# Kernel tuning notes

Hardware: AMD Instinct MI355X
Metric: run time of the kernel (lower is better)

The kernel has to match this reference:

```python
import jax, jax.numpy as jnp
import numpy as np

N_NODES = 50000
N_EDGES = 800000
F_IN, HID, N_CLS = 128, 64, 40
KS = 2  # kernel_size, dim=1, open B-spline, degree=1


def spline_conv(x, src, dst, pseudo, W, root, bias, num_nodes, kernel_size):
    """SplineConv (torch_geometric), dim=1, degree=1, open spline, aggr='mean'."""
    K = kernel_size
    v = pseudo[:, 0] * (K - 1)                       # map [0,1] -> [0, K-1]
    k0 = jnp.clip(jnp.floor(v), 0, K - 2)
    frac = v - k0                                    # linear (degree-1) basis
    i0 = k0.astype(jnp.int32)
    i1 = i0 + 1
    E = src.shape[0]
    e = jnp.arange(E)
    # per-edge kernel coefficients c[e,k] = sum_s basis[e,s]*[idx[e,s]==k]
    c = jnp.zeros((E, K), x.dtype).at[e, i0].add(1.0 - frac).at[e, i1].add(frac)
    xj = x[src]                                      # [E, F_in] gather
    # agg[k] = scatter-add over edges of c[e,k]*xj[e] -> [K, N, F_in]
    agg = jnp.stack([
        jax.ops.segment_sum(c[:, k:k + 1] * xj, dst, num_segments=num_nodes)
        for k in range(K)
    ])
    deg = jax.ops.segment_sum(jnp.ones((E,), x.dtype), dst, num_segments=num_nodes)
    msg = jnp.einsum('kni,kio->no', agg, W) / jnp.maximum(deg, 1.0)[:, None]
    return msg + x @ root + bias


def setup_inputs() -> dict:
    key = jax.random.key(0)
    ks = jax.random.split(key, 9)
    def glorot(k, shape):
        fan_in, fan_out = shape[-2], shape[-1]
        lim = (6.0 / (fan_in + fan_out)) ** 0.5
        return jax.random.uniform(k, shape, jnp.float32, -lim, lim)
    return {
        'x': jax.random.normal(ks[0], (N_NODES, F_IN), jnp.float32),
        'edge_index': jax.random.randint(ks[1], (2, N_EDGES), 0, N_NODES, jnp.int32),
        'edge_attr': jax.random.uniform(ks[2], (N_EDGES, 1), jnp.float32),
        'W1': glorot(ks[3], (KS, F_IN, HID)),
        'root1': glorot(ks[4], (F_IN, HID)),
        'bias1': jnp.zeros((HID,), jnp.float32),
        'W2': glorot(ks[5], (KS, HID, N_CLS)),
        'root2': glorot(ks[6], (HID, N_CLS)),
        'bias2': jnp.zeros((N_CLS,), jnp.float32),
    }


def reference(x, edge_index, edge_attr, W1, root1, bias1, W2, root2, bias2):
    src, dst = edge_index[0], edge_index[1]
    # eval mode: dropout is identity
    h = spline_conv(x, src, dst, edge_attr, W1, root1, bias1, N_NODES, KS)
    h = jax.nn.elu(h)
    out = spline_conv(h, src, dst, edge_attr, W2, root2, bias2, N_NODES, KS)
    return out
```

## Files before the change

### kernel.cpp

```cpp
#include <hip/hip_runtime.h>
#include <math.h>

#define N_NODES 50000
#define N_EDGES 800000
#define F_IN    128
#define HID     64
#define N_CLS   40

#define M1 (3 * HID)
#define M2P 128

#define RANGE_SZ 6250
#define PERM_SLICES 128
#define PERM_CHUNK (N_EDGES / PERM_SLICES)
#define EST 64

#define NW 32768

using sh8 = __attribute__((ext_vector_type(8))) short;
using floatx4 = __attribute__((ext_vector_type(4))) float;

__device__ inline unsigned short f2bf(float f) {
    union { float f; unsigned int u; } c{f};
    unsigned int r = (c.u + 0x7FFF + ((c.u >> 16) & 1)) >> 16;
    return (unsigned short)r;
}
__device__ inline float bf2f(unsigned int u) {
    union { unsigned int u; float f; } c;
    c.u = u << 16;
    return c.f;
}

__global__ void concat_w(const float* __restrict__ W1, const float* __restrict__ root1,
                         const float* __restrict__ W2, const float* __restrict__ root2,
                         unsigned short* __restrict__ WT1, unsigned short* __restrict__ WT2,
                         int* __restrict__ cnt) {
    int i = blockIdx.x * blockDim.x + threadIdx.x;
    if (i < M1 * F_IN) {
        int c = i / F_IN, k = i % F_IN;
        float val;
        if (c < HID)            val = W1[k * HID + c];
        else if (c < 2 * HID)   val = W1[F_IN * HID + k * HID + (c - HID)];
        else                    val = root1[k * HID + (c - 2 * HID)];
        WT1[i] = f2bf(val);
    } else if (i < NW) {
        int ii = i - M1 * F_IN;
        int c = ii / HID, k = ii % HID;
        float val;
        if (c < N_CLS)            val = W2[k * N_CLS + c];
        else if (c < 2 * N_CLS)   val = W2[HID * N_CLS + k * N_CLS + (c - N_CLS)];
        else if (c < 3 * N_CLS)   val = root2[k * N_CLS + (c - 2 * N_CLS)];
        else                      val = 0.0f;
        WT2[ii] = f2bf(val);
    } else {
        int ii = i - NW;
        if (ii < N_NODES) cnt[ii] = 0;
    }
}

template <int KD, bool AF32, int SPLIT, int PW, int ROOTW, int MT>
__device__ __forceinline__ void gemm_body(int bid, const void* __restrict__ Aptr,
                                          const unsigned short* __restrict__ Bt,
                                          unsigned short* __restrict__ Csp,
                                          float* __restrict__ Croot, int Crows) {
    constexpr int KP = KD + 8;
    __shared__ unsigned short As[64 * KP];
    __shared__ unsigned short Bs[64 * KP];

    int tid = threadIdx.x;
    int row0 = bid * 64;

    if (AF32) {
        const float* A = (const float*)Aptr;
        for (int c = tid; c < 64 * (KD / 4); c += 256) {
            int r = c / (KD / 4), q = c % (KD / 4);
            int gr = row0 + r;
            float4 v = make_float4(0.f, 0.f, 0.f, 0.f);
            if (gr < Crows) v = *(const float4*)(A + (size_t)gr * KD + q * 4);
            union { unsigned short s[4]; uint2 u; } pk;
            pk.s[0] = f2bf(v.x); pk.s[1] = f2bf(v.y);
            pk.s[2] = f2bf(v.z); pk.s[3] = f2bf(v.w);
            *(uint2*)&As[r * KP + q * 4] = pk.u;
        }
    } else {
        const unsigned short* A = (const unsigned short*)Aptr;
        for (int c = tid; c < 64 * (KD / 8); c += 256) {
            int r = c / (KD / 8), q = c % (KD / 8);
            int gr = row0 + r;
            sh8 v = {};
            if (gr < Crows) v = *(const sh8*)(A + (size_t)gr * KD + q * 8);
            *(sh8*)&As[r * KP + q * 8] = v;
        }
    }

    int wv = tid >> 6, lane = tid & 63;
    int lrow = lane & 15, lq = lane >> 4;

    for (int mt = 0; mt < MT; ++mt) {
        int c0 = mt * 64;
        __syncthreads();
        for (int c = tid; c < 64 * (KD / 8); c += 256) {
            int r = c / (KD / 8), q = c % (KD / 8);
            *(sh8*)&Bs[r * KP + q * 8] = *(const sh8*)(Bt + (size_t)(c0 + r) * KD + q * 8);
        }
        __syncthreads();

        floatx4 acc[4] = {{0.f,0.f,0.f,0.f},{0.f,0.f,0.f,0.f},{0.f,0.f,0.f,0.f},{0.f,0.f,0.f,0.f}};
#pragma unroll
        for (int kt = 0; kt < KD / 32; ++kt) {
            int kb = kt * 32 + lq * 8;
            sh8 a0 = *(const sh8*)&As[(wv * 16 + lrow) * KP + kb];
#pragma unroll
            for (int cf = 0; cf < 4; ++cf) {
                sh8 b = *(const sh8*)&Bs[(cf * 16 + lrow) * KP + kb];
                acc[cf] = __builtin_amdgcn_mfma_f32_16x16x32_bf16(a0, b, acc[cf], 0, 0, 0);
            }
        }

#pragma unroll
        for (int r = 0; r < 4; ++r) {
            int gr = row0 + wv * 16 + lq * 4 + r;
            if (gr >= Crows) continue;
#pragma unroll
            for (int cf = 0; cf < 4; ++cf) {
                int gc = c0 + cf * 16 + lrow;
                float val = acc[cf][r];
                if (gc < SPLIT) {
                    int pi = (gc < PW) ? gc * 2 : (gc - PW) * 2 + 1;
                    Csp[(size_t)gr * SPLIT + pi] = f2bf(val);
                } else if (gc < SPLIT + ROOTW) {
                    Croot[(size_t)gr * ROOTW + (gc - SPLIT)] = val;
                }
            }
        }
    }
}

__device__ __forceinline__ void permute_body(int b, const int* __restrict__ src,
                                             const int* __restrict__ dst,
                                             const float* __restrict__ attr,
                                             int* __restrict__ cnt,
                                             unsigned int* __restrict__ edata) {
    int range = b & 7;
    int slice = b >> 3;
    int lo = range * RANGE_SZ;
    int e0 = slice * PERM_CHUNK;
    int e1 = e0 + PERM_CHUNK;
    for (int e = e0 + (int)threadIdx.x; e < e1; e += 256) {
        int d = dst[e];
        if ((unsigned)(d - lo) < (unsigned)RANGE_SZ) {
            int pos = atomicAdd(&cnt[d], 1);
            if (pos < EST) {
                unsigned int q = (unsigned int)(attr[e] * 65535.0f + 0.5f);
                edata[d * EST + pos] = (unsigned int)src[e] | (q << 16);
            }
        }
    }
}

__global__ __launch_bounds__(256) void gemm1_permute(const float* __restrict__ x,
                                                     const unsigned short* __restrict__ WT1,
                                                     unsigned short* __restrict__ Ysp,
                                                     float* __restrict__ Yroot,
                                                     const int* __restrict__ src,
                                                     const int* __restrict__ dst,
                                                     const float* __restrict__ attr,
                                                     int* __restrict__ cnt,
                                                     unsigned int* __restrict__ edata,
                                                     int gemmBlocks) {
    if ((int)blockIdx.x < gemmBlocks) {
        gemm_body<128, true, 128, 64, 64, 3>(blockIdx.x, (const void*)x, WT1, Ysp, Yroot, N_NODES);
    } else {
        permute_body(blockIdx.x - gemmBlocks, src, dst, attr, cnt, edata);
    }
}

template <int KD, bool AF32, int SPLIT, int PW, int ROOTW, int MT>
__global__ __launch_bounds__(256) void gemm_mfma(const void* __restrict__ Aptr,
                                                 const unsigned short* __restrict__ Bt,
                                                 unsigned short* __restrict__ Csp,
                                                 float* __restrict__ Croot,
                                                 int Crows) {
    gemm_body<KD, AF32, SPLIT, PW, ROOTW, MT>(blockIdx.x, Aptr, Bt, Csp, Croot, Crows);
}

__global__ __launch_bounds__(256) void gather1(const unsigned short* __restrict__ Ysp,
                                               const float* __restrict__ Yroot,
                                               const int* __restrict__ cnt,
                                               const unsigned int* __restrict__ edata,
                                               const float* __restrict__ bias1,
                                               unsigned short* __restrict__ h) {
    int wave = (blockIdx.x * blockDim.x + threadIdx.x) >> 6;
    int lane = threadIdx.x & 63;
    if (wave >= N_NODES) return;
    int deg = cnt[wave];
    deg = deg > EST ? EST : deg;
    const unsigned int* eb = edata + (size_t)wave * EST;
    const float qs = 1.0f / 65535.0f;
    float acc = 0.0f;
    if (deg <= 16) {
        unsigned int e[16], p[16];
#pragma unroll
        for (int t = 0; t < 16; ++t) e[t] = eb[t];
#pragma unroll
        for (int t = 0; t < 16; ++t) {
            int idx = (t < deg) ? (int)(e[t] & 0xffffu) : 0;
            p[t] = *(const unsigned int*)(Ysp + (size_t)idx * 128 + lane * 2);
        }
#pragma unroll
        for (int t = 0; t < 16; ++t) {
            float m = (t < deg) ? 1.0f : 0.0f;
            float v = (float)(e[t] >> 16) * qs;
            acc += m * ((1.0f - v) * bf2f(p[t] & 0xffffu) + v * bf2f(p[t] >> 16));
        }
    } else {
        unsigned int e[32], p[32];
#pragma unroll
        for (int t = 0; t < 32; ++t) e[t] = eb[t];
#pragma unroll
        for (int t = 0; t < 32; ++t) {
            int idx = (t < deg) ? (int)(e[t] & 0xffffu) : 0;
            p[t] = *(const unsigned int*)(Ysp + (size_t)idx * 128 + lane * 2);
        }
#pragma unroll
        for (int t = 0; t < 32; ++t) {
            float m = (t < deg) ? 1.0f : 0.0f;
            float v = (float)(e[t] >> 16) * qs;
            acc += m * ((1.0f - v) * bf2f(p[t] & 0xffffu) + v * bf2f(p[t] >> 16));
        }
        if (deg > 32) {
            for (int j = 32; j < deg; j += 8) {
                unsigned int e2[8], p2[8];
#pragma unroll
                for (int t = 0; t < 8; ++t) e2[t] = eb[j + t];
#pragma unroll
                for (int t = 0; t < 8; ++t) {
                    int idx = (j + t < deg) ? (int)(e2[t] & 0xffffu) : 0;
                    p2[t] = *(const unsigned int*)(Ysp + (size_t)idx * 128 + lane * 2);
                }
#pragma unroll
                for (int t = 0; t < 8; ++t) {
                    float m = (j + t < deg) ? 1.0f : 0.0f;
                    float v = (float)(e2[t] >> 16) * qs;
                    acc += m * ((1.0f - v) * bf2f(p2[t] & 0xffffu) + v * bf2f(p2[t] >> 16));
                }
            }
        }
    }
    float dg = (float)deg;
    dg = dg > 1.0f ? dg : 1.0f;
    float m = acc / dg + Yroot[(size_t)wave * HID + lane] + bias1[lane];
    m = m > 0.0f ? m : expm1f(m);
    h[(size_t)wave * HID + lane] = f2bf(m);
}

__global__ __launch_bounds__(256) void gather2(const unsigned short* __restrict__ Zsp,
                                               const float* __restrict__ Zroot,
                                               const int* __restrict__ cnt,
                                               const unsigned int* __restrict__ edata,
                                               const float* __restrict__ bias2,
                                               float* __restrict__ out) {
    int wave = (blockIdx.x * blockDim.x + threadIdx.x) >> 6;
    int lane = threadIdx.x & 63;
    if (wave >= N_NODES) return;
    if (lane >= N_CLS) return;
    int deg = cnt[wave];
    deg = deg > EST ? EST : deg;
    const unsigned int* eb = edata + (size_t)wave * EST;
    const float qs = 1.0f / 65535.0f;
    float acc = 0.0f;
    if (deg <= 16) {
        unsigned int e[16], p[16];
#pragma unroll
        for (int t = 0; t < 16; ++t) e[t] = eb[t];
#pragma unroll
        for (int t = 0; t < 16; ++t) {
            int idx = (t < deg) ? (int)(e[t] & 0xffffu) : 0;
            p[t] = *(const unsigned int*)(Zsp + (size_t)idx * 80 + lane * 2);
        }
#pragma unroll
        for (int t = 0; t < 16; ++t) {
            float m = (t < deg) ? 1.0f : 0.0f;
            float v = (float)(e[t] >> 16) * qs;
            acc += m * ((1.0f - v) * bf2f(p[t] & 0xffffu) + v * bf2f(p[t] >> 16));
        }
    } else {
        unsigned int e[32], p[32];
#pragma unroll
        for (int t = 0; t < 32; ++t) e[t] = eb[t];
#pragma unroll
        for (int t = 0; t < 32; ++t) {
            int idx = (t < deg) ? (int)(e[t] & 0xffffu) : 0;
            p[t] = *(const unsigned int*)(Zsp + (size_t)idx * 80 + lane * 2);
        }
#pragma unroll
        for (int t = 0; t < 32; ++t) {
            float m = (t < deg) ? 1.0f : 0.0f;
            float v = (float)(e[t] >> 16) * qs;
            acc += m * ((1.0f - v) * bf2f(p[t] & 0xffffu) + v * bf2f(p[t] >> 16));
        }
        if (deg > 32) {
            for (int j = 32; j < deg; j += 8) {
                unsigned int e2[8], p2[8];
#pragma unroll
                for (int t = 0; t < 8; ++t) e2[t] = eb[j + t];
#pragma unroll
                for (int t = 0; t < 8; ++t) {
                    int idx = (j + t < deg) ? (int)(e2[t] & 0xffffu) : 0;
                    p2[t] = *(const unsigned int*)(Zsp + (size_t)idx * 80 + lane * 2);
                }
#pragma unroll
                for (int t = 0; t < 8; ++t) {
                    float m = (j + t < deg) ? 1.0f : 0.0f;
                    float v = (float)(e2[t] >> 16) * qs;
                    acc += m * ((1.0f - v) * bf2f(p2[t] & 0xffffu) + v * bf2f(p2[t] >> 16));
                }
            }
        }
    }
    float dg = (float)deg;
    dg = dg > 1.0f ? dg : 1.0f;
    out[(size_t)wave * N_CLS + lane] =
        acc / dg + Zroot[(size_t)wave * N_CLS + lane] + bias2[lane];
}

extern "C" void kernel_launch(void* const* d_in, const int* in_sizes, int n_in,
                              void* d_out, int out_size, void* d_ws, size_t ws_size,
                              hipStream_t stream) {
    const float* x     = (const float*)d_in[0];
    const int*   eidx  = (const int*)d_in[1];
    const float* eattr = (const float*)d_in[2];
    const float* W1    = (const float*)d_in[3];
    const float* root1 = (const float*)d_in[4];
    const float* bias1 = (const float*)d_in[5];
    const float* W2    = (const float*)d_in[6];
    const float* root2 = (const float*)d_in[7];
    const float* bias2 = (const float*)d_in[8];
    float* out = (float*)d_out;

    const int* src = eidx;
    const int* dst = eidx + N_EDGES;

    char* base = (char*)d_ws;
    unsigned short* Ysp   = (unsigned short*)base;
    float*          Yroot = (float*)(base + 12800000);
    unsigned short* hb    = (unsigned short*)(base + 25600000);
    unsigned short* WT1   = (unsigned short*)(base + 32000000);
    unsigned short* WT2   = (unsigned short*)(base + 32049152);
    unsigned int*   edata = (unsigned int*)(base + 32065536);
    int*            cnt   = (int*)(base + 44865536);
    unsigned short* Zsp   = Ysp;
    float*          Zroot = Yroot;

    const int GB = (N_NODES + 63) / 64;

    hipLaunchKernelGGL(concat_w, dim3((NW + N_NODES + 255) / 256), dim3(256), 0, stream,
                       W1, root1, W2, root2, WT1, WT2, cnt);

    hipLaunchKernelGGL(gemm1_permute, dim3(GB + 8 * PERM_SLICES), dim3(256), 0, stream,
                       x, WT1, Ysp, Yroot, src, dst, eattr, cnt, edata, GB);
    hipLaunchKernelGGL(gather1, dim3((N_NODES * 64 + 255) / 256), dim3(256), 0, stream,
                       Ysp, Yroot, cnt, edata, bias1, hb);

    hipLaunchKernelGGL((gemm_mfma<64, false, 80, 40, 40, 2>),
                       dim3(GB), dim3(256), 0, stream,
                       (const void*)hb, WT2, Zsp, Zroot, N_NODES);
    hipLaunchKernelGGL(gather2, dim3((N_NODES * 64 + 255) / 256), dim3(256), 0, stream,
                       Zsp, Zroot, cnt, edata, bias2, out);
}
```

Measured before the change: 205.2 us.

## Move edge permute into weight-concat kernel and split GEMM1 out

```diff
diff --git a/kernel.cpp b/kernel.cpp
--- a/kernel.cpp
+++ b/kernel.cpp
@@ -16,6 +16,7 @@
 #define EST 64
 
 #define NW 32768
+#define CW 128
 
 using sh8 = __attribute__((ext_vector_type(8))) short;
 using floatx4 = __attribute__((ext_vector_type(4))) float;
@@ -31,44 +32,64 @@
     return c.f;
 }
 
-__global__ void concat_w(const float* __restrict__ W1, const float* __restrict__ root1,
-                         const float* __restrict__ W2, const float* __restrict__ root2,
-                         unsigned short* __restrict__ WT1, unsigned short* __restrict__ WT2,
-                         int* __restrict__ cnt) {
-    int i = blockIdx.x * blockDim.x + threadIdx.x;
-    if (i < M1 * F_IN) {
-        int c = i / F_IN, k = i % F_IN;
-        float val;
-        if (c < HID)            val = W1[k * HID + c];
-        else if (c < 2 * HID)   val = W1[F_IN * HID + k * HID + (c - HID)];
-        else                    val = root1[k * HID + (c - 2 * HID)];
-        WT1[i] = f2bf(val);
-    } else if (i < NW) {
-        int ii = i - M1 * F_IN;
-        int c = ii / HID, k = ii % HID;
-        float val;
-        if (c < N_CLS)            val = W2[k * N_CLS + c];
-        else if (c < 2 * N_CLS)   val = W2[HID * N_CLS + k * N_CLS + (c - N_CLS)];
-        else if (c < 3 * N_CLS)   val = root2[k * N_CLS + (c - 2 * N_CLS)];
-        else                      val = 0.0f;
-        WT2[ii] = f2bf(val);
+__global__ __launch_bounds__(256) void concat_permute(
+        const float* __restrict__ W1, const float* __restrict__ root1,
+        const float* __restrict__ W2, const float* __restrict__ root2,
+        unsigned short* __restrict__ WT1, unsigned short* __restrict__ WT2,
+        const int* __restrict__ src, const int* __restrict__ dst,
+        const float* __restrict__ attr, int* __restrict__ cnt,
+        unsigned int* __restrict__ edata) {
+    if ((int)blockIdx.x < CW) {
+        int i = blockIdx.x * 256 + threadIdx.x;
+        if (i < M1 * F_IN) {
+            int c = i / F_IN, k = i % F_IN;
+            float val;
+            if (c < HID)            val = W1[k * HID + c];
+            else if (c < 2 * HID)   val = W1[F_IN * HID + k * HID + (c - HID)];
+            else                    val = root1[k * HID + (c - 2 * HID)];
+            WT1[i] = f2bf(val);
+        } else if (i < NW) {
+            int ii = i - M1 * F_IN;
+            int c = ii / HID, k = ii % HID;
+            float val;
+            if (c < N_CLS)            val = W2[k * N_CLS + c];
+            else if (c < 2 * N_CLS)   val = W2[HID * N_CLS + k * N_CLS + (c - N_CLS)];
+            else if (c < 3 * N_CLS)   val = root2[k * N_CLS + (c - 2 * N_CLS)];
+            else                      val = 0.0f;
+            WT2[ii] = f2bf(val);
+        }
     } else {
-        int ii = i - NW;
-        if (ii < N_NODES) cnt[ii] = 0;
+        int b2 = blockIdx.x - CW;
+        int range = b2 & 7;
+        int slice = b2 >> 3;
+        int lo = range * RANGE_SZ;
+        int e0 = slice * PERM_CHUNK;
+        int e1 = e0 + PERM_CHUNK;
+        for (int e = e0 + (int)threadIdx.x; e < e1; e += 256) {
+            int d = dst[e];
+            if ((unsigned)(d - lo) < (unsigned)RANGE_SZ) {
+                int pos = atomicAdd(&cnt[d], 1);
+                if (pos < EST) {
+                    unsigned int q = (unsigned int)(attr[e] * 65535.0f + 0.5f);
+                    edata[d * EST + pos] = (unsigned int)src[e] | (q << 16);
+                }
+            }
+        }
     }
 }
 
 template <int KD, bool AF32, int SPLIT, int PW, int ROOTW, int MT>
-__device__ __forceinline__ void gemm_body(int bid, const void* __restrict__ Aptr,
-                                          const unsigned short* __restrict__ Bt,
-                                          unsigned short* __restrict__ Csp,
-                                          float* __restrict__ Croot, int Crows) {
+__global__ __launch_bounds__(256) void gemm_mfma(const void* __restrict__ Aptr,
+                                                 const unsigned short* __restrict__ Bt,
+                                                 unsigned short* __restrict__ Csp,
+                                                 float* __restrict__ Croot,
+                                                 int Crows) {
     constexpr int KP = KD + 8;
     __shared__ unsigned short As[64 * KP];
     __shared__ unsigned short Bs[64 * KP];
 
     int tid = threadIdx.x;
-    int row0 = bid * 64;
+    int row0 = blockIdx.x * 64;
 
     if (AF32) {
         const float* A = (const float*)Aptr;
@@ -134,54 +155,6 @@
             }
         }
     }
-}
-
-__device__ __forceinline__ void permute_body(int b, const int* __restrict__ src,
-                                             const int* __restrict__ dst,
-                                             const float* __restrict__ attr,
-                                             int* __restrict__ cnt,
-                                             unsigned int* __restrict__ edata) {
-    int range = b & 7;
-    int slice = b >> 3;
-    int lo = range * RANGE_SZ;
-    int e0 = slice * PERM_CHUNK;
-    int e1 = e0 + PERM_CHUNK;
-    for (int e = e0 + (int)threadIdx.x; e < e1; e += 256) {
-        int d = dst[e];
-        if ((unsigned)(d - lo) < (unsigned)RANGE_SZ) {
-            int pos = atomicAdd(&cnt[d], 1);
-            if (pos < EST) {
-                unsigned int q = (unsigned int)(attr[e] * 65535.0f + 0.5f);
-                edata[d * EST + pos] = (unsigned int)src[e] | (q << 16);
-            }
-        }
-    }
-}
-
-__global__ __launch_bounds__(256) void gemm1_permute(const float* __restrict__ x,
-                                                     const unsigned short* __restrict__ WT1,
-                                                     unsigned short* __restrict__ Ysp,
-                                                     float* __restrict__ Yroot,
-                                                     const int* __restrict__ src,
-                                                     const int* __restrict__ dst,
-                                                     const float* __restrict__ attr,
-                                                     int* __restrict__ cnt,
-                                                     unsigned int* __restrict__ edata,
-                                                     int gemmBlocks) {
-    if ((int)blockIdx.x < gemmBlocks) {
-        gemm_body<128, true, 128, 64, 64, 3>(blockIdx.x, (const void*)x, WT1, Ysp, Yroot, N_NODES);
-    } else {
-        permute_body(blockIdx.x - gemmBlocks, src, dst, attr, cnt, edata);
-    }
-}
-
-template <int KD, bool AF32, int SPLIT, int PW, int ROOTW, int MT>
-__global__ __launch_bounds__(256) void gemm_mfma(const void* __restrict__ Aptr,
-                                                 const unsigned short* __restrict__ Bt,
-                                                 unsigned short* __restrict__ Csp,
-                                                 float* __restrict__ Croot,
-                                                 int Crows) {
-    gemm_body<KD, AF32, SPLIT, PW, ROOTW, MT>(blockIdx.x, Aptr, Bt, Csp, Croot, Crows);
 }
 
 __global__ __launch_bounds__(256) void gather1(const unsigned short* __restrict__ Ysp,
@@ -354,11 +327,13 @@
 
     const int GB = (N_NODES + 63) / 64;
 
-    hipLaunchKernelGGL(concat_w, dim3((NW + N_NODES + 255) / 256), dim3(256), 0, stream,
-                       W1, root1, W2, root2, WT1, WT2, cnt);
-
-    hipLaunchKernelGGL(gemm1_permute, dim3(GB + 8 * PERM_SLICES), dim3(256), 0, stream,
-                       x, WT1, Ysp, Yroot, src, dst, eattr, cnt, edata, GB);
+    hipMemsetAsync(cnt, 0, N_NODES * sizeof(int), stream);
+    hipLaunchKernelGGL(concat_permute, dim3(CW + 8 * PERM_SLICES), dim3(256), 0, stream,
+                       W1, root1, W2, root2, WT1, WT2, src, dst, eattr, cnt, edata);
+
+    hipLaunchKernelGGL((gemm_mfma<128, true, 128, 64, 64, 3>),
+                       dim3(GB), dim3(256), 0, stream,
+                       (const void*)x, WT1, Ysp, Yroot, N_NODES);
     hipLaunchKernelGGL(gather1, dim3((N_NODES * 64 + 255) / 256), dim3(256), 0, stream,
                        Ysp, Yroot, cnt, edata, bias1, hb);
 
```

New measurement: 209.1 us. Within noise of the previous version (+1.9%).

## Scan each edge once in permute, add nontemporal loads, memset counters

Applied to the files above, without the earlier changes.

```diff
diff --git a/kernel.cpp b/kernel.cpp
--- a/kernel.cpp
+++ b/kernel.cpp
@@ -10,9 +10,8 @@
 #define M1 (3 * HID)
 #define M2P 128
 
-#define RANGE_SZ 6250
-#define PERM_SLICES 128
-#define PERM_CHUNK (N_EDGES / PERM_SLICES)
+#define PERM_CHUNK 782
+#define PERM_BLOCKS ((N_EDGES + PERM_CHUNK - 1) / PERM_CHUNK)
 #define EST 64
 
 #define NW 32768
@@ -33,8 +32,7 @@
 
 __global__ void concat_w(const float* __restrict__ W1, const float* __restrict__ root1,
                          const float* __restrict__ W2, const float* __restrict__ root2,
-                         unsigned short* __restrict__ WT1, unsigned short* __restrict__ WT2,
-                         int* __restrict__ cnt) {
+                         unsigned short* __restrict__ WT1, unsigned short* __restrict__ WT2) {
     int i = blockIdx.x * blockDim.x + threadIdx.x;
     if (i < M1 * F_IN) {
         int c = i / F_IN, k = i % F_IN;
@@ -52,9 +50,6 @@
         else if (c < 3 * N_CLS)   val = root2[k * N_CLS + (c - 2 * N_CLS)];
         else                      val = 0.0f;
         WT2[ii] = f2bf(val);
-    } else {
-        int ii = i - NW;
-        if (ii < N_NODES) cnt[ii] = 0;
     }
 }
 
@@ -141,18 +136,30 @@
                                              const float* __restrict__ attr,
                                              int* __restrict__ cnt,
                                              unsigned int* __restrict__ edata) {
-    int range = b & 7;
-    int slice = b >> 3;
-    int lo = range * RANGE_SZ;
-    int e0 = slice * PERM_CHUNK;
+    int e0 = b * PERM_CHUNK;
     int e1 = e0 + PERM_CHUNK;
-    for (int e = e0 + (int)threadIdx.x; e < e1; e += 256) {
-        int d = dst[e];
-        if ((unsigned)(d - lo) < (unsigned)RANGE_SZ) {
-            int pos = atomicAdd(&cnt[d], 1);
+    if (e1 > N_EDGES) e1 = N_EDGES;
+    for (int e = e0 + (int)threadIdx.x; e < e1; e += 512) {
+        int eB = e + 256;
+        bool okB = eB < e1;
+        int dA = __builtin_nontemporal_load(&dst[e]);
+        int dB = okB ? __builtin_nontemporal_load(&dst[eB]) : 0;
+        int sA = __builtin_nontemporal_load(&src[e]);
+        int sB = okB ? __builtin_nontemporal_load(&src[eB]) : 0;
+        float aA = __builtin_nontemporal_load(&attr[e]);
+        float aB = okB ? __builtin_nontemporal_load(&attr[eB]) : 0.0f;
+        {
+            int pos = atomicAdd(&cnt[dA], 1);
             if (pos < EST) {
-                unsigned int q = (unsigned int)(attr[e] * 65535.0f + 0.5f);
-                edata[d * EST + pos] = (unsigned int)src[e] | (q << 16);
+                unsigned int q = (unsigned int)(aA * 65535.0f + 0.5f);
+                edata[dA * EST + pos] = (unsigned int)sA | (q << 16);
+            }
+        }
+        if (okB) {
+            int pos = atomicAdd(&cnt[dB], 1);
+            if (pos < EST) {
+                unsigned int q = (unsigned int)(aB * 65535.0f + 0.5f);
+                edata[dB * EST + pos] = (unsigned int)sB | (q << 16);
             }
         }
     }
@@ -201,7 +208,7 @@
     if (deg <= 16) {
         unsigned int e[16], p[16];
 #pragma unroll
-        for (int t = 0; t < 16; ++t) e[t] = eb[t];
+        for (int t = 0; t < 16; ++t) e[t] = __builtin_nontemporal_load(&eb[t]);
 #pragma unroll
         for (int t = 0; t < 16; ++t) {
             int idx = (t < deg) ? (int)(e[t] & 0xffffu) : 0;
@@ -216,7 +223,7 @@
     } else {
         unsigned int e[32], p[32];
 #pragma unroll
-        for (int t = 0; t < 32; ++t) e[t] = eb[t];
+        for (int t = 0; t < 32; ++t) e[t] = __builtin_nontemporal_load(&eb[t]);
 #pragma unroll
         for (int t = 0; t < 32; ++t) {
             int idx = (t < deg) ? (int)(e[t] & 0xffffu) : 0;
@@ -272,7 +279,7 @@
     if (deg <= 16) {
         unsigned int e[16], p[16];
 #pragma unroll
-        for (int t = 0; t < 16; ++t) e[t] = eb[t];
+        for (int t = 0; t < 16; ++t) e[t] = __builtin_nontemporal_load(&eb[t]);
 #pragma unroll
         for (int t = 0; t < 16; ++t) {
             int idx = (t < deg) ? (int)(e[t] & 0xffffu) : 0;
@@ -287,7 +294,7 @@
     } else {
         unsigned int e[32], p[32];
 #pragma unroll
-        for (int t = 0; t < 32; ++t) e[t] = eb[t];
+        for (int t = 0; t < 32; ++t) e[t] = __builtin_nontemporal_load(&eb[t]);
 #pragma unroll
         for (int t = 0; t < 32; ++t) {
             int idx = (t < deg) ? (int)(e[t] & 0xffffu) : 0;
@@ -354,10 +361,11 @@
 
     const int GB = (N_NODES + 63) / 64;
 
-    hipLaunchKernelGGL(concat_w, dim3((NW + N_NODES + 255) / 256), dim3(256), 0, stream,
-                       W1, root1, W2, root2, WT1, WT2, cnt);
-
-    hipLaunchKernelGGL(gemm1_permute, dim3(GB + 8 * PERM_SLICES), dim3(256), 0, stream,
+    hipMemsetAsync(cnt, 0, N_NODES * sizeof(int), stream);
+    hipLaunchKernelGGL(concat_w, dim3((NW + 255) / 256), dim3(256), 0, stream,
+                       W1, root1, W2, root2, WT1, WT2);
+
+    hipLaunchKernelGGL(gemm1_permute, dim3(GB + PERM_BLOCKS), dim3(256), 0, stream,
                        x, WT1, Ysp, Yroot, src, dst, eattr, cnt, edata, GB);
     hipLaunchKernelGGL(gather1, dim3((N_NODES * 64 + 255) / 256), dim3(256), 0, stream,
                        Ysp, Yroot, cnt, edata, bias1, hb);
```

New measurement: 206.4 us. About the same (+0.5%).
